# Kernel tuning notes

Measured on AMD Instinct MI355X. Metric: run time of the kernel, lower is better.

## Reference

```python
import jax, jax.numpy as jnp
import numpy as np

B, T, E = 2, 2048, 1024   # batch, block_size, emb_d
H, D = 16, 64             # heads, head_size


def setup_inputs() -> dict:
    key = jax.random.key(0)
    ks = jax.random.split(key, 7)
    s = 1.0 / np.sqrt(E)
    inputs = jax.random.normal(ks[0], (B, T, E), dtype=jnp.float32)
    k_w = jax.random.uniform(ks[1], (H, E, D), jnp.float32, -s, s)
    k_b = jax.random.uniform(ks[2], (H, D), jnp.float32, -s, s)
    q_w = jax.random.uniform(ks[3], (H, E, D), jnp.float32, -s, s)
    q_b = jax.random.uniform(ks[4], (H, D), jnp.float32, -s, s)
    v_w = jax.random.uniform(ks[5], (H, E, D), jnp.float32, -s, s)
    v_b = jax.random.uniform(ks[6], (H, D), jnp.float32, -s, s)
    return {"inputs": inputs, "k_w": k_w, "k_b": k_b,
            "q_w": q_w, "q_b": q_b, "v_w": v_w, "v_b": v_b}


def reference(inputs, k_w, k_b, q_w, q_b, v_w, v_b):
    # Per-head linear projections, vectorized over heads: (B,T,E)x(H,E,D)->(B,H,T,D)
    k = jnp.einsum('bte,hed->bhtd', inputs, k_w) + k_b[None, :, None, :]
    q = jnp.einsum('bte,hed->bhtd', inputs, q_w) + q_b[None, :, None, :]
    v = jnp.einsum('bte,hed->bhtd', inputs, v_w) + v_b[None, :, None, :]

    scale = D ** (-0.5)
    # scores: (B,H,Tq,Tk)
    w = jnp.einsum('bhtd,bhsd->bhts', q, k) * scale
    tril = jnp.tril(jnp.ones((T, T), dtype=bool))
    w = jnp.where(tril[None, None, :, :], w, -jnp.inf)
    # NOTE: original torch code does softmax(weights, dim=1) on a (B,T,T)
    # tensor, i.e. over the QUERY axis. Faithfully reproduce: axis=-2 here.
    w = jax.nn.softmax(w, axis=-2)
    out = jnp.einsum('bhts,bhsd->bhtd', w, v)           # (B,H,T,D)
    # concat heads along last dim, head-major order matching torch.cat
    return out.transpose(0, 2, 1, 3).reshape(B, T, H * D)
```

## Files before the change

### kernel.cpp

```cpp
#include <hip/hip_runtime.h>
#include <hip/hip_bf16.h>
#include <math.h>

#define B_ 2
#define T_ 2048
#define E_ 1024
#define H_ 16
#define D_ 64
#define NT_ 32

typedef __attribute__((ext_vector_type(8))) short bf16x8;
typedef __attribute__((ext_vector_type(4))) float f32x4;

__device__ __forceinline__ unsigned short f2bf(float x) {
  union { float f; unsigned u; } v; v.f = x;
  unsigned r = v.u + 0x7FFFu + ((v.u >> 16) & 1u);
  return (unsigned short)(r >> 16);
}
__device__ __forceinline__ float bf2f(unsigned short u) {
  union { float f; unsigned u; } v; v.u = ((unsigned)u) << 16; return v.f;
}
__device__ __forceinline__ unsigned pk2bf(float a, float b) {
  return (unsigned)f2bf(a) | ((unsigned)f2bf(b) << 16);
}

__device__ __forceinline__ void dma8(const unsigned short* g, int gstride,
                                     unsigned short* l, int lane)
{
  const int r = lane >> 3, bg = (lane & 7) ^ (r & 7);
  __builtin_amdgcn_global_load_lds(
      (const __attribute__((address_space(1))) void*)(g + (size_t)r * gstride + bg * 8),
      (__attribute__((address_space(3))) void*)l, 16, 0, 0);
}
__device__ __forceinline__ bf16x8 frag(const unsigned short* tile, int row, int g) {
  return *(const bf16x8*)(tile + row * 64 + (((g ^ row) & 7) << 3));
}

__global__ __launch_bounds__(256) void inpack_kernel(const float* __restrict__ in,
                                                     unsigned short* __restrict__ o) {
  const size_t i = ((size_t)blockIdx.x * 256 + threadIdx.x) * 8;
  float4 f0 = *(const float4*)(in + i);
  float4 f1 = *(const float4*)(in + i + 4);
  unsigned u[4] = { pk2bf(f0.x, f0.y), pk2bf(f0.z, f0.w),
                    pk2bf(f1.x, f1.y), pk2bf(f1.z, f1.w) };
  *(bf16x8*)(o + i) = *(const bf16x8*)u;
}

__global__ __launch_bounds__(256) void wpack_kernel(
    const float* __restrict__ qw, const float* __restrict__ kw, const float* __restrict__ vw,
    unsigned short* __restrict__ qwt, unsigned short* __restrict__ kwt,
    unsigned short* __restrict__ vwt)
{
  __shared__ float s[64][65];
  const int tid = threadIdx.x;
  const int e0 = blockIdx.x * 64, h = blockIdx.y, z = blockIdx.z;
  const float* w = (z == 0) ? qw : (z == 1) ? kw : vw;
  unsigned short* o = (z == 0) ? qwt : (z == 1) ? kwt : vwt;
  {
    const int r = tid >> 2;
    #pragma unroll
    for (int p = 0; p < 4; ++p) {
      const int c = (tid & 3) * 4 + p * 16;
      float4 f = *(const float4*)(w + ((size_t)(h * E_ + e0 + r)) * D_ + c);
      s[r][c] = f.x; s[r][c+1] = f.y; s[r][c+2] = f.z; s[r][c+3] = f.w;
    }
  }
  __syncthreads();
  {
    const int d = tid >> 2, ec = (tid & 3) * 16;
    unsigned short tmp[16];
    #pragma unroll
    for (int j = 0; j < 16; ++j) tmp[j] = f2bf(s[ec + j][d]);
    unsigned short* dst = o + ((size_t)(h * D_ + d)) * E_ + e0 + ec;
    *(bf16x8*)(dst)     = *(const bf16x8*)&tmp[0];
    *(bf16x8*)(dst + 8) = *(const bf16x8*)&tmp[8];
  }
}

__global__ __launch_bounds__(256) void proj_kernel(
    const unsigned short* __restrict__ in16,
    const unsigned short* __restrict__ qwt, const unsigned short* __restrict__ kwt,
    const unsigned short* __restrict__ vwt,
    const float* __restrict__ qb, const float* __restrict__ kb, const float* __restrict__ vb,
    unsigned short* __restrict__ qo, unsigned short* __restrict__ ko,
    unsigned short* __restrict__ vo)
{
  __shared__ __align__(16) unsigned short in_s[2][128 * 64];
  __shared__ __align__(16) unsigned short w_s[2][3][64 * 64];
  const int tid = threadIdx.x;
  const int lane = tid & 63, wv = tid >> 6;
  const int l15 = lane & 15, quad = lane >> 4;
  const int t0 = blockIdx.x * 128, h = blockIdx.y, b = blockIdx.z;
  const unsigned short* wts[3] = { qwt, kwt, vwt };

  f32x4 acc[3][2][4];
  #pragma unroll
  for (int x = 0; x < 3; ++x)
    #pragma unroll
    for (int s = 0; s < 2; ++s)
      #pragma unroll
      for (int nb = 0; nb < 4; ++nb) acc[x][s][nb] = (f32x4){0.f, 0.f, 0.f, 0.f};

#define PROJ_STAGE(e0_, bi_)                                                      \
  {                                                                               \
    const unsigned short* gin = in16 + ((size_t)(b * T_ + t0)) * E_ + (e0_);      \
    _Pragma("unroll")                                                             \
    for (int p = 0; p < 4; ++p) {                                                 \
      const int br = wv * 32 + p * 8;                                             \
      dma8(gin + (size_t)br * E_, E_, &in_s[bi_][br * 64], lane);                 \
    }                                                                             \
    _Pragma("unroll")                                                             \
    for (int j = 0; j < 6; ++j) {                                                 \
      const int idx = wv * 6 + j;                                                 \
      const int x = idx >> 3, br = (idx & 7) * 8;                                 \
      dma8(wts[x] + ((size_t)(h * D_ + br)) * E_ + (e0_), E_,                     \
           &w_s[bi_][x][br * 64], lane);                                          \
    }                                                                             \
  }

  PROJ_STAGE(0, 0);
  __syncthreads();
  for (int e = 0; e < 16; ++e) {
    const int bi = e & 1;
    if (e < 15) PROJ_STAGE((e + 1) * 64, bi ^ 1);
    const unsigned short* is = in_s[bi];
    #pragma unroll
    for (int kk = 0; kk < 2; ++kk) {
      const int g0 = kk * 4 + quad;
      bf16x8 a0 = frag(is, wv * 32 + l15, g0);
      bf16x8 a1 = frag(is, wv * 32 + 16 + l15, g0);
      #pragma unroll
      for (int x = 0; x < 3; ++x) {
        const unsigned short* ws = w_s[bi][x];
        #pragma unroll
        for (int nb = 0; nb < 4; ++nb) {
          bf16x8 bfr = frag(ws, nb * 16 + l15, g0);
          acc[x][0][nb] = __builtin_amdgcn_mfma_f32_16x16x32_bf16(a0, bfr, acc[x][0][nb], 0, 0, 0);
          acc[x][1][nb] = __builtin_amdgcn_mfma_f32_16x16x32_bf16(a1, bfr, acc[x][1][nb], 0, 0, 0);
        }
      }
    }
    __syncthreads();
  }
#undef PROJ_STAGE

  const size_t obase = (size_t)(b * H_ + h) * T_;
  unsigned short* outs[3] = { qo, ko, vo };
  const float* biasp[3] = { qb, kb, vb };
  #pragma unroll
  for (int x = 0; x < 3; ++x) {
    #pragma unroll
    for (int nb = 0; nb < 4; ++nb) {
      const int d = nb * 16 + l15;
      const float bvv = biasp[x][h * D_ + d];
      #pragma unroll
      for (int s = 0; s < 2; ++s)
        #pragma unroll
        for (int r = 0; r < 4; ++r) {
          const int t = t0 + wv * 32 + s * 16 + quad * 4 + r;
          outs[x][(obase + t) * D_ + d] = f2bf(acc[x][s][nb][r] + bvv);
        }
    }
  }
}

__global__ __launch_bounds__(256) void stats_kernel(
    const unsigned short* __restrict__ q, const unsigned short* __restrict__ k,
    const unsigned short* __restrict__ v, unsigned short* __restrict__ vt)
{
  __shared__ __align__(16) unsigned short k_s[2][64 * 64];
  __shared__ __align__(16) unsigned short q_s[2][64 * 64];
  __shared__ float red[4][2][64];
  __shared__ float rl_sh[2][64];
  const int tid = threadIdx.x;
  const int lane = tid & 63, wv = tid >> 6;
  const int l15 = lane & 15, quad = lane >> 4;
  const int x = blockIdx.x;
  const int bh = blockIdx.z * H_ + blockIdx.y;
  const int sa = x, sb = 31 - x;
  const int s0a = sa * 64, s0b = sb * 64;

  #pragma unroll
  for (int j = 0; j < 4; ++j) {
    const int idx = wv * 4 + j;
    const int tl = idx >> 3, br = (idx & 7) * 8;
    dma8(k + ((size_t)(bh * T_ + (tl ? s0b : s0a) + br)) * 64, 64,
         &k_s[tl][br * 64], lane);
  }
  #pragma unroll
  for (int p = 0; p < 2; ++p) {
    const int br = wv * 16 + p * 8;
    dma8(q + ((size_t)(bh * T_ + s0a + br)) * 64, 64, &q_s[0][br * 64], lane);
  }
  __syncthreads();

  bf16x8 kf[2][4][2];
  #pragma unroll
  for (int tl = 0; tl < 2; ++tl)
    #pragma unroll
    for (int nb = 0; nb < 4; ++nb)
      #pragma unroll
      for (int kk = 0; kk < 2; ++kk)
        kf[tl][nb][kk] = frag(k_s[tl], nb * 16 + l15, kk * 4 + quad);

  float lsum[2][4];
  #pragma unroll
  for (int tl = 0; tl < 2; ++tl)
    #pragma unroll
    for (int nb = 0; nb < 4; ++nb) lsum[tl][nb] = 0.f;

  for (int tt = sa; tt < NT_; ++tt) {
    const int bi = (tt - sa) & 1;
    if (tt < NT_ - 1) {
      #pragma unroll
      for (int p = 0; p < 2; ++p) {
        const int br = wv * 16 + p * 8;
        dma8(q + ((size_t)(bh * T_ + (tt + 1) * 64 + br)) * 64, 64,
             &q_s[bi ^ 1][br * 64], lane);
      }
    }
    bf16x8 a0 = frag(q_s[bi], wv * 16 + l15, quad);
    bf16x8 a1 = frag(q_s[bi], wv * 16 + l15, 4 + quad);
    const int tbase = tt * 64 + wv * 16 + quad * 4;
    {
      f32x4 sacc[4];
      #pragma unroll
      for (int nb = 0; nb < 4; ++nb) sacc[nb] = (f32x4){0.f, 0.f, 0.f, 0.f};
      #pragma unroll
      for (int nb = 0; nb < 4; ++nb) {
        sacc[nb] = __builtin_amdgcn_mfma_f32_16x16x32_bf16(a0, kf[0][nb][0], sacc[nb], 0, 0, 0);
        sacc[nb] = __builtin_amdgcn_mfma_f32_16x16x32_bf16(a1, kf[0][nb][1], sacc[nb], 0, 0, 0);
      }
      #pragma unroll
      for (int nb = 0; nb < 4; ++nb) {
        const int s = s0a + nb * 16 + l15;
        #pragma unroll
        for (int r = 0; r < 4; ++r)
          lsum[0][nb] += (tbase + r >= s) ? __expf(sacc[nb][r] * 0.125f) : 0.f;
      }
    }
    if (tt >= sb) {
      f32x4 sacc[4];
      #pragma unroll
      for (int nb = 0; nb < 4; ++nb) sacc[nb] = (f32x4){0.f, 0.f, 0.f, 0.f};
      #pragma unroll
      for (int nb = 0; nb < 4; ++nb) {
        sacc[nb] = __builtin_amdgcn_mfma_f32_16x16x32_bf16(a0, kf[1][nb][0], sacc[nb], 0, 0, 0);
        sacc[nb] = __builtin_amdgcn_mfma_f32_16x16x32_bf16(a1, kf[1][nb][1], sacc[nb], 0, 0, 0);
      }
      #pragma unroll
      for (int nb = 0; nb < 4; ++nb) {
        const int s = s0b + nb * 16 + l15;
        #pragma unroll
        for (int r = 0; r < 4; ++r)
          lsum[1][nb] += (tbase + r >= s) ? __expf(sacc[nb][r] * 0.125f) : 0.f;
      }
    }
    __syncthreads();
  }

  #pragma unroll
  for (int tl = 0; tl < 2; ++tl)
    #pragma unroll
    for (int nb = 0; nb < 4; ++nb) {
      lsum[tl][nb] += __shfl_xor(lsum[tl][nb], 16);
      lsum[tl][nb] += __shfl_xor(lsum[tl][nb], 32);
    }
  if (lane < 16) {
    #pragma unroll
    for (int tl = 0; tl < 2; ++tl)
      #pragma unroll
      for (int nb = 0; nb < 4; ++nb) red[wv][tl][nb * 16 + lane] = lsum[tl][nb];
  }
  __syncthreads();
  if (tid < 128) {
    const int tl = tid >> 6, sL = tid & 63;
    const float L = red[0][tl][sL] + red[1][tl][sL] + red[2][tl][sL] + red[3][tl][sL];
    rl_sh[tl][sL] = 1.0f / L;
  }
  __syncthreads();
  #pragma unroll
  for (int tl = 0; tl < 2; ++tl) {
    const int s0 = tl ? s0b : s0a;
    const int sI = tid >> 2, c = (tid & 3) * 16;
    const unsigned short* gv = v + ((size_t)(bh * T_ + s0 + sI)) * 64 + c;
    bf16x8 v0 = *(const bf16x8*)gv;
    bf16x8 v1 = *(const bf16x8*)(gv + 8);
    const float r = rl_sh[tl][sI];
    #pragma unroll
    for (int j = 0; j < 8; ++j)
      vt[((size_t)(bh * D_ + c + j)) * T_ + s0 + sI] = f2bf(bf2f((unsigned short)v0[j]) * r);
    #pragma unroll
    for (int j = 0; j < 8; ++j)
      vt[((size_t)(bh * D_ + c + 8 + j)) * T_ + s0 + sI] = f2bf(bf2f((unsigned short)v1[j]) * r);
  }
}

__global__ __launch_bounds__(256) void out_kernel(
    const unsigned short* __restrict__ q, const unsigned short* __restrict__ k,
    const unsigned short* __restrict__ vt, float* __restrict__ out)
{
  __shared__ __align__(16) unsigned short q_s[2][64 * 64];
  __shared__ __align__(16) unsigned short k_s[2][64 * 64];
  __shared__ __align__(16) unsigned short vt_s[2][64 * 64];
  __shared__ __align__(16) unsigned short u_s[2][64 * 72];
  const int tid = threadIdx.x;
  const int lane = tid & 63, wv = tid >> 6;
  const int l15 = lane & 15, quad = lane >> 4;
  const int xp = blockIdx.x;
  const int bh = blockIdx.z * H_ + blockIdx.y;
  const int ja = xp, jb = 31 - xp;
  const int t0a = ja * 64, t0b = jb * 64;

  #pragma unroll
  for (int j = 0; j < 4; ++j) {
    const int idx = wv * 4 + j;
    const int tl = idx >> 3, br = (idx & 7) * 8;
    dma8(q + ((size_t)(bh * T_ + (tl ? t0b : t0a) + br)) * 64, 64,
         &q_s[tl][br * 64], lane);
  }
  #pragma unroll
  for (int p = 0; p < 2; ++p) {
    const int br = wv * 16 + p * 8;
    dma8(k + ((size_t)(bh * T_ + br)) * 64, 64, &k_s[0][br * 64], lane);
    dma8(vt + ((size_t)(bh * D_ + br)) * T_, T_, &vt_s[0][br * 64], lane);
  }
  __syncthreads();

  bf16x8 qf[2][2];
  #pragma unroll
  for (int tl = 0; tl < 2; ++tl)
    #pragma unroll
    for (int kk = 0; kk < 2; ++kk)
      qf[tl][kk] = frag(q_s[tl], wv * 16 + l15, kk * 4 + quad);
  __syncthreads();

  f32x4 oacc[2][4];
  #pragma unroll
  for (int tl = 0; tl < 2; ++tl)
    #pragma unroll
    for (int nb = 0; nb < 4; ++nb) oacc[tl][nb] = (f32x4){0.f, 0.f, 0.f, 0.f};

  for (int st = 0; st <= jb; ++st) {
    const int bi = st & 1;
    if (st < jb) {
      const int s1 = (st + 1) * 64;
      #pragma unroll
      for (int p = 0; p < 2; ++p) {
        const int br = wv * 16 + p * 8;
        dma8(k + ((size_t)(bh * T_ + s1 + br)) * 64, 64, &k_s[bi ^ 1][br * 64], lane);
        dma8(vt + ((size_t)(bh * D_ + br)) * T_ + s1, T_, &vt_s[bi ^ 1][br * 64], lane);
      }
    }
    const int s0 = st * 64;
    const unsigned short* ks = k_s[bi];
    const unsigned short* vs = vt_s[bi];
    bf16x8 kfA[4][2];
    #pragma unroll
    for (int mb = 0; mb < 4; ++mb)
      #pragma unroll
      for (int kk = 0; kk < 2; ++kk)
        kfA[mb][kk] = frag(ks, mb * 16 + l15, kk * 4 + quad);

    #pragma unroll
    for (int ti = 0; ti < 2; ++ti) {
      if (ti == 0 && st > ja) continue;
      const int t0 = ti ? t0b : t0a;
      const int tcol = t0 + wv * 16 + l15;
      f32x4 sacc[4];
      #pragma unroll
      for (int mb = 0; mb < 4; ++mb) sacc[mb] = (f32x4){0.f, 0.f, 0.f, 0.f};
      #pragma unroll
      for (int mb = 0; mb < 4; ++mb) {
        sacc[mb] = __builtin_amdgcn_mfma_f32_16x16x32_bf16(kfA[mb][0], qf[ti][0], sacc[mb], 0, 0, 0);
        sacc[mb] = __builtin_amdgcn_mfma_f32_16x16x32_bf16(kfA[mb][1], qf[ti][1], sacc[mb], 0, 0, 0);
      }
      unsigned short* urow = &u_s[ti][(wv * 16 + l15) * 72];
      #pragma unroll
      for (int mb = 0; mb < 4; ++mb) {
        const int sbase = s0 + mb * 16 + quad * 4;
        float uu[4];
        #pragma unroll
        for (int r = 0; r < 4; ++r)
          uu[r] = (tcol >= sbase + r) ? __expf(sacc[mb][r] * 0.125f) : 0.f;
        *(uint2*)(urow + mb * 16 + quad * 4) =
            make_uint2(pk2bf(uu[0], uu[1]), pk2bf(uu[2], uu[3]));
      }
      #pragma unroll
      for (int kk = 0; kk < 2; ++kk) {
        bf16x8 ua = *(const bf16x8*)(&u_s[ti][(wv * 16 + l15) * 72 + kk * 32 + quad * 8]);
        #pragma unroll
        for (int nb = 0; nb < 4; ++nb)
          oacc[ti][nb] = __builtin_amdgcn_mfma_f32_16x16x32_bf16(
              ua, frag(vs, nb * 16 + l15, kk * 4 + quad), oacc[ti][nb], 0, 0, 0);
      }
    }
    __syncthreads();
  }
  #pragma unroll
  for (int ti = 0; ti < 2; ++ti) {
    const int t0 = ti ? t0b : t0a;
    #pragma unroll
    for (int nb = 0; nb < 4; ++nb) {
      const int d = nb * 16 + l15;
      #pragma unroll
      for (int r = 0; r < 4; ++r) {
        const int t = t0 + wv * 16 + quad * 4 + r;
        out[((size_t)(blockIdx.z * T_ + t)) * (H_ * D_) + blockIdx.y * D_ + d] = oacc[ti][nb][r];
      }
    }
  }
}

extern "C" void kernel_launch(void* const* d_in, const int* in_sizes, int n_in,
                              void* d_out, int out_size, void* d_ws, size_t ws_size,
                              hipStream_t stream) {
  const float* in = (const float*)d_in[0];
  const float* kw = (const float*)d_in[1];
  const float* kb = (const float*)d_in[2];
  const float* qw = (const float*)d_in[3];
  const float* qb = (const float*)d_in[4];
  const float* vw = (const float*)d_in[5];
  const float* vb = (const float*)d_in[6];
  float* out = (float*)d_out;

  unsigned short* p = (unsigned short*)d_ws;
  const size_t inz = (size_t)B_ * T_ * E_;
  const size_t wz  = (size_t)H_ * D_ * E_;
  const size_t qz  = (size_t)B_ * H_ * T_ * D_;
  unsigned short* in16 = p;            p += inz;
  unsigned short* qwt  = p;            p += wz;
  unsigned short* kwt  = p;            p += wz;
  unsigned short* vwt  = p;            p += wz;
  unsigned short* q16  = p;            p += qz;
  unsigned short* k16  = p;            p += qz;
  unsigned short* v16  = p;            p += qz;
  unsigned short* vtb  = p;            p += qz;

  dim3 blk(256);
  inpack_kernel<<<dim3(inz / 2048), blk, 0, stream>>>(in, in16);
  wpack_kernel <<<dim3(E_ / 64, H_, 3), blk, 0, stream>>>(qw, kw, vw, qwt, kwt, vwt);
  proj_kernel  <<<dim3(T_ / 128, H_, B_), blk, 0, stream>>>(in16, qwt, kwt, vwt,
                                                            qb, kb, vb, q16, k16, v16);
  stats_kernel <<<dim3(16, H_, B_), blk, 0, stream>>>(q16, k16, v16, vtb);
  out_kernel   <<<dim3(16, H_, B_), blk, 0, stream>>>(q16, k16, vtb, out);
}
```

Before: 192.5 us.

## Drop LDS staging and pairing in attention kernels, fold scale into Q with exp2

Stats and output kernels stop pairing two tiles per block. They now launch one 64-row tile per block, doubling the grid. They also drop the double-buffered LDS staging and the per-iteration barriers, loading K/Q/V fragments straight from global memory into registers. The softmax scale and log2(e) are folded into Q at projection time so the inner loops use a raw exp2 and apply the causal mask only on the diagonal tile. This gives more parallelism and less sync and ALU work, but risks poorer load coalescing and latency hiding without LDS reuse, plus unbalanced per-block work.

```diff
diff --git a/kernel.cpp b/kernel.cpp
--- a/kernel.cpp
+++ b/kernel.cpp
@@ -8,9 +8,16 @@
 #define H_ 16
 #define D_ 64
 #define NT_ 32
+#define QSCALE 0.180336880f
 
 typedef __attribute__((ext_vector_type(8))) short bf16x8;
 typedef __attribute__((ext_vector_type(4))) float f32x4;
+
+#if __has_builtin(__builtin_amdgcn_exp2f)
+#define EXP2(x) __builtin_amdgcn_exp2f(x)
+#else
+#define EXP2(x) exp2f(x)
+#endif
 
 __device__ __forceinline__ unsigned short f2bf(float x) {
   union { float f; unsigned u; } v; v.f = x;
@@ -21,7 +28,8 @@
   union { float f; unsigned u; } v; v.u = ((unsigned)u) << 16; return v.f;
 }
 __device__ __forceinline__ unsigned pk2bf(float a, float b) {
-  return (unsigned)f2bf(a) | ((unsigned)f2bf(b) << 16);
+  __hip_bfloat162 h = __float22bfloat162_rn(make_float2(a, b));
+  union { __hip_bfloat162 h; unsigned u; } c; c.h = h; return c.u;
 }
 
 __device__ __forceinline__ void dma8(const unsigned short* g, int gstride,
@@ -149,6 +157,7 @@
   const float* biasp[3] = { qb, kb, vb };
   #pragma unroll
   for (int x = 0; x < 3; ++x) {
+    const float scl = (x == 0) ? QSCALE : 1.0f;
     #pragma unroll
     for (int nb = 0; nb < 4; ++nb) {
       const int d = nb * 16 + l15;
@@ -158,7 +167,7 @@
         #pragma unroll
         for (int r = 0; r < 4; ++r) {
           const int t = t0 + wv * 32 + s * 16 + quad * 4 + r;
-          outs[x][(obase + t) * D_ + d] = f2bf(acc[x][s][nb][r] + bvv);
+          outs[x][(obase + t) * D_ + d] = f2bf((acc[x][s][nb][r] + bvv) * scl);
         }
     }
   }
@@ -168,125 +177,73 @@
     const unsigned short* __restrict__ q, const unsigned short* __restrict__ k,
     const unsigned short* __restrict__ v, unsigned short* __restrict__ vt)
 {
-  __shared__ __align__(16) unsigned short k_s[2][64 * 64];
-  __shared__ __align__(16) unsigned short q_s[2][64 * 64];
-  __shared__ float red[4][2][64];
-  __shared__ float rl_sh[2][64];
+  __shared__ float red[4][64];
+  __shared__ float rl_sh[64];
   const int tid = threadIdx.x;
   const int lane = tid & 63, wv = tid >> 6;
   const int l15 = lane & 15, quad = lane >> 4;
-  const int x = blockIdx.x;
+  const int sa = blockIdx.x;
   const int bh = blockIdx.z * H_ + blockIdx.y;
-  const int sa = x, sb = 31 - x;
-  const int s0a = sa * 64, s0b = sb * 64;
-
-  #pragma unroll
-  for (int j = 0; j < 4; ++j) {
-    const int idx = wv * 4 + j;
-    const int tl = idx >> 3, br = (idx & 7) * 8;
-    dma8(k + ((size_t)(bh * T_ + (tl ? s0b : s0a) + br)) * 64, 64,
-         &k_s[tl][br * 64], lane);
-  }
-  #pragma unroll
-  for (int p = 0; p < 2; ++p) {
-    const int br = wv * 16 + p * 8;
-    dma8(q + ((size_t)(bh * T_ + s0a + br)) * 64, 64, &q_s[0][br * 64], lane);
+  const int s0 = sa * 64;
+  const unsigned short* kbase = k + (size_t)bh * T_ * 64;
+  const unsigned short* qbase = q + (size_t)bh * T_ * 64;
+
+  bf16x8 kf[4][2];
+  #pragma unroll
+  for (int nb = 0; nb < 4; ++nb)
+    #pragma unroll
+    for (int kk = 0; kk < 2; ++kk)
+      kf[nb][kk] = *(const bf16x8*)(kbase + (size_t)(s0 + nb * 16 + l15) * 64 + kk * 32 + quad * 8);
+
+  float lsum[4] = {0.f, 0.f, 0.f, 0.f};
+
+  for (int tt = sa; tt < NT_; ++tt) {
+    const unsigned short* qrow = qbase + (size_t)(tt * 64 + wv * 16 + l15) * 64;
+    bf16x8 a0 = *(const bf16x8*)(qrow + quad * 8);
+    bf16x8 a1 = *(const bf16x8*)(qrow + 32 + quad * 8);
+    f32x4 sacc[4];
+    #pragma unroll
+    for (int nb = 0; nb < 4; ++nb) sacc[nb] = (f32x4){0.f, 0.f, 0.f, 0.f};
+    #pragma unroll
+    for (int nb = 0; nb < 4; ++nb) {
+      sacc[nb] = __builtin_amdgcn_mfma_f32_16x16x32_bf16(a0, kf[nb][0], sacc[nb], 0, 0, 0);
+      sacc[nb] = __builtin_amdgcn_mfma_f32_16x16x32_bf16(a1, kf[nb][1], sacc[nb], 0, 0, 0);
+    }
+    if (tt == sa) {
+      const int tbase = tt * 64 + wv * 16 + quad * 4;
+      #pragma unroll
+      for (int nb = 0; nb < 4; ++nb) {
+        const int s = s0 + nb * 16 + l15;
+        #pragma unroll
+        for (int r = 0; r < 4; ++r)
+          lsum[nb] += (tbase + r >= s) ? EXP2(sacc[nb][r]) : 0.f;
+      }
+    } else {
+      #pragma unroll
+      for (int nb = 0; nb < 4; ++nb)
+        #pragma unroll
+        for (int r = 0; r < 4; ++r) lsum[nb] += EXP2(sacc[nb][r]);
+    }
+  }
+  #pragma unroll
+  for (int nb = 0; nb < 4; ++nb) {
+    lsum[nb] += __shfl_xor(lsum[nb], 16);
+    lsum[nb] += __shfl_xor(lsum[nb], 32);
+  }
+  if (lane < 16) {
+    #pragma unroll
+    for (int nb = 0; nb < 4; ++nb) red[wv][nb * 16 + lane] = lsum[nb];
   }
   __syncthreads();
-
-  bf16x8 kf[2][4][2];
-  #pragma unroll
-  for (int tl = 0; tl < 2; ++tl)
-    #pragma unroll
-    for (int nb = 0; nb < 4; ++nb)
-      #pragma unroll
-      for (int kk = 0; kk < 2; ++kk)
-        kf[tl][nb][kk] = frag(k_s[tl], nb * 16 + l15, kk * 4 + quad);
-
-  float lsum[2][4];
-  #pragma unroll
-  for (int tl = 0; tl < 2; ++tl)
-    #pragma unroll
-    for (int nb = 0; nb < 4; ++nb) lsum[tl][nb] = 0.f;
-
-  for (int tt = sa; tt < NT_; ++tt) {
-    const int bi = (tt - sa) & 1;
-    if (tt < NT_ - 1) {
-      #pragma unroll
-      for (int p = 0; p < 2; ++p) {
-        const int br = wv * 16 + p * 8;
-        dma8(q + ((size_t)(bh * T_ + (tt + 1) * 64 + br)) * 64, 64,
-             &q_s[bi ^ 1][br * 64], lane);
-      }
-    }
-    bf16x8 a0 = frag(q_s[bi], wv * 16 + l15, quad);
-    bf16x8 a1 = frag(q_s[bi], wv * 16 + l15, 4 + quad);
-    const int tbase = tt * 64 + wv * 16 + quad * 4;
-    {
-      f32x4 sacc[4];
-      #pragma unroll
-      for (int nb = 0; nb < 4; ++nb) sacc[nb] = (f32x4){0.f, 0.f, 0.f, 0.f};
-      #pragma unroll
-      for (int nb = 0; nb < 4; ++nb) {
-        sacc[nb] = __builtin_amdgcn_mfma_f32_16x16x32_bf16(a0, kf[0][nb][0], sacc[nb], 0, 0, 0);
-        sacc[nb] = __builtin_amdgcn_mfma_f32_16x16x32_bf16(a1, kf[0][nb][1], sacc[nb], 0, 0, 0);
-      }
-      #pragma unroll
-      for (int nb = 0; nb < 4; ++nb) {
-        const int s = s0a + nb * 16 + l15;
-        #pragma unroll
-        for (int r = 0; r < 4; ++r)
-          lsum[0][nb] += (tbase + r >= s) ? __expf(sacc[nb][r] * 0.125f) : 0.f;
-      }
-    }
-    if (tt >= sb) {
-      f32x4 sacc[4];
-      #pragma unroll
-      for (int nb = 0; nb < 4; ++nb) sacc[nb] = (f32x4){0.f, 0.f, 0.f, 0.f};
-      #pragma unroll
-      for (int nb = 0; nb < 4; ++nb) {
-        sacc[nb] = __builtin_amdgcn_mfma_f32_16x16x32_bf16(a0, kf[1][nb][0], sacc[nb], 0, 0, 0);
-        sacc[nb] = __builtin_amdgcn_mfma_f32_16x16x32_bf16(a1, kf[1][nb][1], sacc[nb], 0, 0, 0);
-      }
-      #pragma unroll
-      for (int nb = 0; nb < 4; ++nb) {
-        const int s = s0b + nb * 16 + l15;
-        #pragma unroll
-        for (int r = 0; r < 4; ++r)
-          lsum[1][nb] += (tbase + r >= s) ? __expf(sacc[nb][r] * 0.125f) : 0.f;
-      }
-    }
-    __syncthreads();
-  }
-
-  #pragma unroll
-  for (int tl = 0; tl < 2; ++tl)
-    #pragma unroll
-    for (int nb = 0; nb < 4; ++nb) {
-      lsum[tl][nb] += __shfl_xor(lsum[tl][nb], 16);
-      lsum[tl][nb] += __shfl_xor(lsum[tl][nb], 32);
-    }
-  if (lane < 16) {
-    #pragma unroll
-    for (int tl = 0; tl < 2; ++tl)
-      #pragma unroll
-      for (int nb = 0; nb < 4; ++nb) red[wv][tl][nb * 16 + lane] = lsum[tl][nb];
-  }
+  if (tid < 64)
+    rl_sh[tid] = 1.0f / (red[0][tid] + red[1][tid] + red[2][tid] + red[3][tid]);
   __syncthreads();
-  if (tid < 128) {
-    const int tl = tid >> 6, sL = tid & 63;
-    const float L = red[0][tl][sL] + red[1][tl][sL] + red[2][tl][sL] + red[3][tl][sL];
-    rl_sh[tl][sL] = 1.0f / L;
-  }
-  __syncthreads();
-  #pragma unroll
-  for (int tl = 0; tl < 2; ++tl) {
-    const int s0 = tl ? s0b : s0a;
+  {
     const int sI = tid >> 2, c = (tid & 3) * 16;
     const unsigned short* gv = v + ((size_t)(bh * T_ + s0 + sI)) * 64 + c;
     bf16x8 v0 = *(const bf16x8*)gv;
     bf16x8 v1 = *(const bf16x8*)(gv + 8);
-    const float r = rl_sh[tl][sI];
+    const float r = rl_sh[sI];
     #pragma unroll
     for (int j = 0; j < 8; ++j)
       vt[((size_t)(bh * D_ + c + j)) * T_ + s0 + sI] = f2bf(bf2f((unsigned short)v0[j]) * r);
@@ -300,114 +257,78 @@
     const unsigned short* __restrict__ q, const unsigned short* __restrict__ k,
     const unsigned short* __restrict__ vt, float* __restrict__ out)
 {
-  __shared__ __align__(16) unsigned short q_s[2][64 * 64];
-  __shared__ __align__(16) unsigned short k_s[2][64 * 64];
-  __shared__ __align__(16) unsigned short vt_s[2][64 * 64];
-  __shared__ __align__(16) unsigned short u_s[2][64 * 72];
+  __shared__ __align__(16) unsigned short u_s[4][16][72];
   const int tid = threadIdx.x;
   const int lane = tid & 63, wv = tid >> 6;
   const int l15 = lane & 15, quad = lane >> 4;
-  const int xp = blockIdx.x;
+  const int jt = 31 - blockIdx.x;
   const int bh = blockIdx.z * H_ + blockIdx.y;
-  const int ja = xp, jb = 31 - xp;
-  const int t0a = ja * 64, t0b = jb * 64;
-
-  #pragma unroll
-  for (int j = 0; j < 4; ++j) {
-    const int idx = wv * 4 + j;
-    const int tl = idx >> 3, br = (idx & 7) * 8;
-    dma8(q + ((size_t)(bh * T_ + (tl ? t0b : t0a) + br)) * 64, 64,
-         &q_s[tl][br * 64], lane);
-  }
-  #pragma unroll
-  for (int p = 0; p < 2; ++p) {
-    const int br = wv * 16 + p * 8;
-    dma8(k + ((size_t)(bh * T_ + br)) * 64, 64, &k_s[0][br * 64], lane);
-    dma8(vt + ((size_t)(bh * D_ + br)) * T_, T_, &vt_s[0][br * 64], lane);
-  }
-  __syncthreads();
-
-  bf16x8 qf[2][2];
-  #pragma unroll
-  for (int tl = 0; tl < 2; ++tl)
-    #pragma unroll
-    for (int kk = 0; kk < 2; ++kk)
-      qf[tl][kk] = frag(q_s[tl], wv * 16 + l15, kk * 4 + quad);
-  __syncthreads();
-
-  f32x4 oacc[2][4];
-  #pragma unroll
-  for (int tl = 0; tl < 2; ++tl)
-    #pragma unroll
-    for (int nb = 0; nb < 4; ++nb) oacc[tl][nb] = (f32x4){0.f, 0.f, 0.f, 0.f};
-
-  for (int st = 0; st <= jb; ++st) {
-    const int bi = st & 1;
-    if (st < jb) {
-      const int s1 = (st + 1) * 64;
-      #pragma unroll
-      for (int p = 0; p < 2; ++p) {
-        const int br = wv * 16 + p * 8;
-        dma8(k + ((size_t)(bh * T_ + s1 + br)) * 64, 64, &k_s[bi ^ 1][br * 64], lane);
-        dma8(vt + ((size_t)(bh * D_ + br)) * T_ + s1, T_, &vt_s[bi ^ 1][br * 64], lane);
-      }
-    }
+  const int t0 = jt * 64;
+  const unsigned short* kbase = k + (size_t)bh * T_ * 64;
+  const unsigned short* vbase = vt + (size_t)bh * D_ * T_;
+
+  const unsigned short* qrow = q + (size_t)(bh * T_ + t0 + wv * 16 + l15) * 64;
+  bf16x8 qf0 = *(const bf16x8*)(qrow + quad * 8);
+  bf16x8 qf1 = *(const bf16x8*)(qrow + 32 + quad * 8);
+
+  f32x4 oacc[4];
+  #pragma unroll
+  for (int nb = 0; nb < 4; ++nb) oacc[nb] = (f32x4){0.f, 0.f, 0.f, 0.f};
+
+  unsigned short* urow = &u_s[wv][l15][0];
+  const int tcol = t0 + wv * 16 + l15;
+
+  for (int st = 0; st <= jt; ++st) {
     const int s0 = st * 64;
-    const unsigned short* ks = k_s[bi];
-    const unsigned short* vs = vt_s[bi];
-    bf16x8 kfA[4][2];
-    #pragma unroll
-    for (int mb = 0; mb < 4; ++mb)
-      #pragma unroll
-      for (int kk = 0; kk < 2; ++kk)
-        kfA[mb][kk] = frag(ks, mb * 16 + l15, kk * 4 + quad);
-
-    #pragma unroll
-    for (int ti = 0; ti < 2; ++ti) {
-      if (ti == 0 && st > ja) continue;
-      const int t0 = ti ? t0b : t0a;
-      const int tcol = t0 + wv * 16 + l15;
-      f32x4 sacc[4];
-      #pragma unroll
-      for (int mb = 0; mb < 4; ++mb) sacc[mb] = (f32x4){0.f, 0.f, 0.f, 0.f};
-      #pragma unroll
-      for (int mb = 0; mb < 4; ++mb) {
-        sacc[mb] = __builtin_amdgcn_mfma_f32_16x16x32_bf16(kfA[mb][0], qf[ti][0], sacc[mb], 0, 0, 0);
-        sacc[mb] = __builtin_amdgcn_mfma_f32_16x16x32_bf16(kfA[mb][1], qf[ti][1], sacc[mb], 0, 0, 0);
-      }
-      unsigned short* urow = &u_s[ti][(wv * 16 + l15) * 72];
+    f32x4 sacc[4];
+    #pragma unroll
+    for (int mb = 0; mb < 4; ++mb) sacc[mb] = (f32x4){0.f, 0.f, 0.f, 0.f};
+    #pragma unroll
+    for (int mb = 0; mb < 4; ++mb) {
+      const unsigned short* krow = kbase + (size_t)(s0 + mb * 16 + l15) * 64;
+      bf16x8 ka0 = *(const bf16x8*)(krow + quad * 8);
+      bf16x8 ka1 = *(const bf16x8*)(krow + 32 + quad * 8);
+      sacc[mb] = __builtin_amdgcn_mfma_f32_16x16x32_bf16(ka0, qf0, sacc[mb], 0, 0, 0);
+      sacc[mb] = __builtin_amdgcn_mfma_f32_16x16x32_bf16(ka1, qf1, sacc[mb], 0, 0, 0);
+    }
+    if (st == jt) {
       #pragma unroll
       for (int mb = 0; mb < 4; ++mb) {
         const int sbase = s0 + mb * 16 + quad * 4;
         float uu[4];
         #pragma unroll
         for (int r = 0; r < 4; ++r)
-          uu[r] = (tcol >= sbase + r) ? __expf(sacc[mb][r] * 0.125f) : 0.f;
+          uu[r] = (tcol >= sbase + r) ? EXP2(sacc[mb][r]) : 0.f;
         *(uint2*)(urow + mb * 16 + quad * 4) =
             make_uint2(pk2bf(uu[0], uu[1]), pk2bf(uu[2], uu[3]));
       }
-      #pragma unroll
-      for (int kk = 0; kk < 2; ++kk) {
-        bf16x8 ua = *(const bf16x8*)(&u_s[ti][(wv * 16 + l15) * 72 + kk * 32 + quad * 8]);
-        #pragma unroll
-        for (int nb = 0; nb < 4; ++nb)
-          oacc[ti][nb] = __builtin_amdgcn_mfma_f32_16x16x32_bf16(
-              ua, frag(vs, nb * 16 + l15, kk * 4 + quad), oacc[ti][nb], 0, 0, 0);
-      }
-    }
-    __syncthreads();
-  }
-  #pragma unroll
-  for (int ti = 0; ti < 2; ++ti) {
-    const int t0 = ti ? t0b : t0a;
-    #pragma unroll
-    for (int nb = 0; nb < 4; ++nb) {
-      const int d = nb * 16 + l15;
-      #pragma unroll
-      for (int r = 0; r < 4; ++r) {
-        const int t = t0 + wv * 16 + quad * 4 + r;
-        out[((size_t)(blockIdx.z * T_ + t)) * (H_ * D_) + blockIdx.y * D_ + d] = oacc[ti][nb][r];
-      }
+    } else {
+      #pragma unroll
+      for (int mb = 0; mb < 4; ++mb) {
+        float uu[4];
+        #pragma unroll
+        for (int r = 0; r < 4; ++r) uu[r] = EXP2(sacc[mb][r]);
+        *(uint2*)(urow + mb * 16 + quad * 4) =
+            make_uint2(pk2bf(uu[0], uu[1]), pk2bf(uu[2], uu[3]));
+      }
+    }
+    #pragma unroll
+    for (int kk = 0; kk < 2; ++kk) {
+      bf16x8 ua = *(const bf16x8*)(urow + kk * 32 + quad * 8);
+      #pragma unroll
+      for (int nb = 0; nb < 4; ++nb) {
+        bf16x8 vb = *(const bf16x8*)(vbase + (size_t)(nb * 16 + l15) * T_ + s0 + kk * 32 + quad * 8);
+        oacc[nb] = __builtin_amdgcn_mfma_f32_16x16x32_bf16(ua, vb, oacc[nb], 0, 0, 0);
+      }
+    }
+  }
+  #pragma unroll
+  for (int nb = 0; nb < 4; ++nb) {
+    const int d = nb * 16 + l15;
+    #pragma unroll
+    for (int r = 0; r < 4; ++r) {
+      const int t = t0 + wv * 16 + quad * 4 + r;
+      out[((size_t)(blockIdx.z * T_ + t)) * (H_ * D_) + blockIdx.y * D_ + d] = oacc[nb][r];
     }
   }
 }
@@ -442,6 +363,6 @@
   wpack_kernel <<<dim3(E_ / 64, H_, 3), blk, 0, stream>>>(qw, kw, vw, qwt, kwt, vwt);
   proj_kernel  <<<dim3(T_ / 128, H_, B_), blk, 0, stream>>>(in16, qwt, kwt, vwt,
                                                             qb, kb, vb, q16, k16, v16);
-  stats_kernel <<<dim3(16, H_, B_), blk, 0, stream>>>(q16, k16, v16, vtb);
-  out_kernel   <<<dim3(16, H_, B_), blk, 0, stream>>>(q16, k16, vtb, out);
-}
+  stats_kernel <<<dim3(NT_, H_, B_), blk, 0, stream>>>(q16, k16, v16, vtb);
+  out_kernel   <<<dim3(NT_, H_, B_), blk, 0, stream>>>(q16, k16, vtb, out);
+}
```

Result: slower. 380.9 us (+97.9%).
